# Kernel tuning notes

Hardware: AMD Instinct MI355X
Metric: run time of the kernel (lower is better)

Reference implementation:

```python
import jax, jax.numpy as jnp
import numpy as np

NH = 4  # num_heads
P = 8   # EDFFN patch size


def conv1x1(x, w):
    # x: (B,C,H,W), w: (O,C)
    return jnp.einsum('bchw,oc->bohw', x, w)


def dwconv3x3(x, w):
    # depthwise 3x3, SAME padding. x: (B,C,H,W), w: (C,1,3,3)
    return jax.lax.conv_general_dilated(
        x, w, window_strides=(1, 1), padding='SAME',
        dimension_numbers=('NCHW', 'OIHW', 'NCHW'),
        feature_group_count=x.shape[1])


def affine(x, s, b):
    # folded BatchNorm (eval mode): per-channel scale + bias
    return x * s[None, :, None, None] + b[None, :, None, None]


def setup_inputs() -> dict:
    key = jax.random.key(0)
    ks = jax.random.split(key, 10)
    B, C, H, W = 16, 256, 32, 32
    hd = C // NH              # 64
    kd = hd // 2              # 32 (attn_ratio=0.5)
    h_qkv = C + 2 * kd * NH   # 512
    hid = 2 * C               # EDFFN hidden_features = 512
    x = jax.random.normal(ks[0], (B, C, H, W), dtype=jnp.float32)
    d = {
        'x': x,
        # Attention (ultralytics Conv = conv(no bias) + BN folded to scale/bias)
        'qkv_w': jax.random.normal(ks[1], (h_qkv, C), jnp.float32) * 0.05,
        'qkv_s': jnp.ones((h_qkv,), jnp.float32),
        'qkv_b': jnp.zeros((h_qkv,), jnp.float32),
        'pe_w': jax.random.normal(ks[2], (C, 1, 3, 3), jnp.float32) * 0.1,
        'pe_s': jnp.ones((C,), jnp.float32),
        'pe_b': jnp.zeros((C,), jnp.float32),
        'proj_w': jax.random.normal(ks[3], (C, C), jnp.float32) * 0.05,
        'proj_s': jnp.ones((C,), jnp.float32),
        'proj_b': jnp.zeros((C,), jnp.float32),
        # EDFFN (plain Conv2d, bias=False)
        'pin_w': jax.random.normal(ks[4], (2 * hid, C), jnp.float32) * 0.05,
        'dw_w': jax.random.normal(ks[5], (2 * hid, 1, 3, 3), jnp.float32) * 0.1,
        'fft_filt': jnp.ones((C, 1, 1, P, P // 2 + 1), jnp.float32),
        'pout_w': jax.random.normal(ks[6], (C, hid), jnp.float32) * 0.05,
    }
    return d


def reference(x, qkv_w, qkv_s, qkv_b, pe_w, pe_s, pe_b, proj_w, proj_s, proj_b,
              pin_w, dw_w, fft_filt, pout_w):
    B, C, H, W = x.shape
    hd = C // NH
    kd = hd // 2
    scale = kd ** -0.5
    N = H * W

    # ---- Attention ----
    qkv = affine(conv1x1(x, qkv_w), qkv_s, qkv_b)          # (B, C+2*NH*kd, H, W)
    qkv = qkv.reshape(B, NH, 2 * kd + hd, N)
    q = qkv[:, :, :kd]              # (B, NH, kd, N)
    k = qkv[:, :, kd:2 * kd]        # (B, NH, kd, N)
    v = qkv[:, :, 2 * kd:]          # (B, NH, hd, N)
    attn = jnp.einsum('bhcn,bhcm->bhnm', q, k) * scale     # q^T @ k
    attn = jax.nn.softmax(attn, axis=-1)
    out = jnp.einsum('bhdm,bhnm->bhdn', v, attn)           # v @ attn^T
    out = out.reshape(B, C, H, W)
    v_img = v.reshape(B, C, H, W)
    pe = affine(dwconv3x3(v_img, pe_w), pe_s, pe_b)
    a = affine(conv1x1(out + pe, proj_w), proj_s, proj_b)
    x = x + a                                               # shortcut

    # ---- EDFFN ----
    y = conv1x1(x, pin_w)                                   # (B, 4C, H, W)
    y = dwconv3x3(y, dw_w)
    y1, y2 = jnp.split(y, 2, axis=1)
    y = jax.nn.gelu(y1, approximate=False) * y2             # (B, 2C, H, W)
    y = conv1x1(y, pout_w)                                  # (B, C, H, W)
    h_n = (-H) % P
    w_n = (-W) % P
    if h_n or w_n:
        y = jnp.pad(y, ((0, 0), (0, 0), (0, h_n), (0, w_n)), mode='reflect')
    Hp, Wp = y.shape[2], y.shape[3]
    # (B,C,Hp/P,P,Wp/P,P) -> (B,C,Hp/P,Wp/P,P,P)
    yp = y.reshape(B, C, Hp // P, P, Wp // P, P).transpose(0, 1, 2, 4, 3, 5)
    yf = jnp.fft.rfft2(yp.astype(jnp.float32)) * fft_filt   # filter broadcast (C,1,1,P,P//2+1)
    yp = jnp.fft.irfft2(yf, s=(P, P))
    y = yp.transpose(0, 1, 2, 4, 3, 5).reshape(B, C, Hp, Wp)[:, :, :H, :W]
    return x + y                                            # shortcut
```

## Files before the change

### kernel.cpp

```cpp
#include <hip/hip_runtime.h>
#include <math.h>

#define NPIX 1024

typedef __bf16 bf16x8 __attribute__((ext_vector_type(8)));
typedef float  f32x4  __attribute__((ext_vector_type(4)));

__global__ __launch_bounds__(256) void conv1x1_mfma_kernel(
    const float* __restrict__ in, const float* __restrict__ W,
    const float* __restrict__ sc, const float* __restrict__ bi,
    const float* __restrict__ res, float* __restrict__ out,
    int O, int C) {
  const int b  = blockIdx.z;
  const int o0 = blockIdx.y << 7;
  const int n0 = blockIdx.x << 7;
  const float* inb  = in  + (size_t)b * C * NPIX;
  float*       outb = out + (size_t)b * O * NPIX;
  const float* resb = res ? res + (size_t)b * O * NPIX : nullptr;

  __shared__ __align__(16) __bf16 a_s[128][40];
  __shared__ __align__(16) __bf16 b_s[128][40];

  const int t    = threadIdx.x;
  const int lane = t & 63;
  const int wv   = t >> 6;
  const int wo   = (wv >> 1) << 6;
  const int wn   = (wv & 1) << 6;
  const int lr   = lane & 15;
  const int g    = lane >> 4;

  const int ao = t >> 1, ak = (t & 1) << 4;
  const int bn = t & 127, bk = (t >> 7) << 4;
  const float* wrow = &W[(size_t)(o0 + ao) * C];

  f32x4 acc[4][4];
#pragma unroll
  for (int m = 0; m < 4; ++m)
#pragma unroll
    for (int n = 0; n < 4; ++n) acc[m][n] = (f32x4){0.f, 0.f, 0.f, 0.f};

  for (int k0 = 0; k0 < C; k0 += 32) {
    __syncthreads();
    {
      const float* wp = wrow + k0 + ak;
#pragma unroll
      for (int half = 0; half < 2; ++half) {
        float4 lo = *(const float4*)&wp[half * 8];
        float4 hi = *(const float4*)&wp[half * 8 + 4];
        union { __bf16 h[8]; uint4 u; } pk;
        pk.h[0] = (__bf16)lo.x; pk.h[1] = (__bf16)lo.y;
        pk.h[2] = (__bf16)lo.z; pk.h[3] = (__bf16)lo.w;
        pk.h[4] = (__bf16)hi.x; pk.h[5] = (__bf16)hi.y;
        pk.h[6] = (__bf16)hi.z; pk.h[7] = (__bf16)hi.w;
        *(uint4*)((char*)&a_s[ao][ak] + half * 16) = pk.u;
      }
    }
    {
#pragma unroll
      for (int p = 0; p < 4; ++p) {
        const int kk = k0 + bk + (p << 2);
        union { __bf16 h[4]; uint2 u; } pk;
        pk.h[0] = (__bf16)inb[(size_t)(kk + 0) * NPIX + n0 + bn];
        pk.h[1] = (__bf16)inb[(size_t)(kk + 1) * NPIX + n0 + bn];
        pk.h[2] = (__bf16)inb[(size_t)(kk + 2) * NPIX + n0 + bn];
        pk.h[3] = (__bf16)inb[(size_t)(kk + 3) * NPIX + n0 + bn];
        *(uint2*)((char*)&b_s[bn][bk] + (p << 3)) = pk.u;
      }
    }
    __syncthreads();
    bf16x8 af[4], bfr[4];
#pragma unroll
    for (int m = 0; m < 4; ++m)
      af[m] = *(const bf16x8*)((const char*)&a_s[wo + (m << 4) + lr][0] + (g << 4));
#pragma unroll
    for (int n = 0; n < 4; ++n)
      bfr[n] = *(const bf16x8*)((const char*)&b_s[wn + (n << 4) + lr][0] + (g << 4));
#pragma unroll
    for (int m = 0; m < 4; ++m)
#pragma unroll
      for (int n = 0; n < 4; ++n)
        acc[m][n] = __builtin_amdgcn_mfma_f32_16x16x32_bf16(
            af[m], bfr[n], acc[m][n], 0, 0, 0);
  }

#pragma unroll
  for (int m = 0; m < 4; ++m) {
#pragma unroll
    for (int r = 0; r < 4; ++r) {
      const int o = o0 + wo + (m << 4) + (g << 2) + r;
      const float s  = sc ? sc[o] : 1.f;
      const float bb = bi ? bi[o] : 0.f;
      float* orow = &outb[(size_t)o * NPIX];
      const float* rrow = resb ? &resb[(size_t)o * NPIX] : nullptr;
#pragma unroll
      for (int n = 0; n < 4; ++n) {
        const int nn = n0 + wn + (n << 4) + lr;
        float v = fmaf(acc[m][n][r], s, bb);
        if (rrow) v += rrow[nn];
        orow[nn] = v;
      }
    }
  }
}

__global__ __launch_bounds__(256) void attn_mfma_kernel(
    const float* __restrict__ qkv, float* __restrict__ outbuf) {
  const int L    = blockIdx.x;
  const int xcd  = L & 7;
  const int rrr  = L >> 3;
  const int tile = rrr & 15;
  const int bh   = xcd + ((rrr >> 4) << 3);
  const int h    = bh & 3;
  const int b    = bh >> 2;
  const int n0   = tile << 6;
  const float scale = 0.1767766952966369f;
  const float* base = qkv + ((size_t)b * 512 + h * 128) * NPIX;

  __shared__ __align__(16) char kt_b[64 * 128];
  __shared__ __align__(16) char v_b[64 * 128];
  __shared__ __align__(16) char p_b[4 * 16 * 128];

  const int t    = threadIdx.x;
  const int w    = t >> 6;
  const int lane = t & 63;
  const int lq   = lane & 15;
  const int g    = lane >> 4;

  bf16x8 qf;
  {
    const float* qp = base + (size_t)(g << 3) * NPIX + n0 + (w << 4) + lq;
#pragma unroll
    for (int j = 0; j < 8; ++j)
      qf[j] = (__bf16)(qp[(size_t)j * NPIX] * scale);
  }

  const int cp = t >> 4;
  const int rq = t & 15;
  const float* kr0 = base + (size_t)(32 + (cp << 1)) * NPIX;
  const float* kr1 = kr0 + NPIX;
  const int koff = (cp << 2) ^ ((rq & 7) << 4);
  const int vn = t & 15;
  const int vr = t >> 4;
  const float* vrp = base + (size_t)(64 + vr) * NPIX;

  char* pw = p_b + (w << 11);
  const int pswz = (lq & 7) << 4;

  float m_run = -3.0e38f, l_run = 0.f;
  f32x4 acc0 = {0.f, 0.f, 0.f, 0.f}, acc1 = acc0, acc2 = acc0, acc3 = acc0;

  for (int mt = 0; mt < 16; ++mt) {
    const int m0 = mt << 6;
    __syncthreads();
#pragma unroll
    for (int i = 0; i < 4; ++i) {
      const int m = rq + (i << 4);
      union { __bf16 h2[2]; unsigned u; } pk;
      pk.h2[0] = (__bf16)kr0[m0 + m];
      pk.h2[1] = (__bf16)kr1[m0 + m];
      *(unsigned*)(kt_b + (m << 7) + koff) = pk.u;
    }
#pragma unroll
    for (int i = 0; i < 4; ++i) {
      const int vd = vr + (i << 4);
      float4 v4 = *(const float4*)&vrp[(size_t)(i << 4) * NPIX + m0 + (vn << 2)];
      union { __bf16 h[4]; uint2 u; } pk;
      pk.h[0] = (__bf16)v4.x; pk.h[1] = (__bf16)v4.y;
      pk.h[2] = (__bf16)v4.z; pk.h[3] = (__bf16)v4.w;
      *(uint2*)(v_b + (vd << 7) + ((vn << 3) ^ ((vd & 7) << 4))) = pk.u;
    }
    __syncthreads();

    f32x4 st[4];
#pragma unroll
    for (int tt = 0; tt < 4; ++tt) {
      const int m = (tt << 4) + lq;
      const bf16x8 kfrag = *(const bf16x8*)(
          kt_b + (m << 7) + ((g ^ (lq & 7)) << 4));
      st[tt] = __builtin_amdgcn_mfma_f32_16x16x32_bf16(
          kfrag, qf, (f32x4){0.f, 0.f, 0.f, 0.f}, 0, 0, 0);
    }

    float tmax = -3.0e38f;
#pragma unroll
    for (int tt = 0; tt < 4; ++tt)
#pragma unroll
      for (int r = 0; r < 4; ++r) tmax = fmaxf(tmax, st[tt][r]);
    tmax = fmaxf(tmax, __shfl_xor(tmax, 16));
    tmax = fmaxf(tmax, __shfl_xor(tmax, 32));
    const float mnew  = fmaxf(m_run, tmax);
    const float alpha = __expf(m_run - mnew);
    float ssum = 0.f;
#pragma unroll
    for (int tt = 0; tt < 4; ++tt)
#pragma unroll
      for (int r = 0; r < 4; ++r) {
        st[tt][r] = __expf(st[tt][r] - mnew);
        ssum += st[tt][r];
      }
    ssum += __shfl_xor(ssum, 16);
    ssum += __shfl_xor(ssum, 32);
    l_run = l_run * alpha + ssum;
    m_run = mnew;
    acc0 *= alpha; acc1 *= alpha; acc2 *= alpha; acc3 *= alpha;

#pragma unroll
    for (int tt = 0; tt < 4; ++tt) {
      union { __bf16 h[4]; uint2 u; } pk;
      pk.h[0] = (__bf16)st[tt][0]; pk.h[1] = (__bf16)st[tt][1];
      pk.h[2] = (__bf16)st[tt][2]; pk.h[3] = (__bf16)st[tt][3];
      *(uint2*)(pw + (lq << 7) + (((tt << 5) + (g << 3)) ^ pswz)) = pk.u;
    }

#pragma unroll
    for (int s = 0; s < 2; ++s) {
      const bf16x8 pf = *(const bf16x8*)(
          pw + (lq << 7) + (((s << 6) + (g << 4)) ^ pswz));
      const int cb = ((g << 4) + (s << 6));
#pragma unroll
      for (int dt = 0; dt < 4; ++dt) {
        const int row = (dt << 4) + lq;
        const bf16x8 vfrag = *(const bf16x8*)(
            v_b + (row << 7) + (cb ^ ((lq & 7) << 4)));
        f32x4& a = (dt == 0) ? acc0 : (dt == 1) ? acc1 : (dt == 2) ? acc2 : acc3;
        a = __builtin_amdgcn_mfma_f32_16x16x32_bf16(vfrag, pf, a, 0, 0, 0);
      }
    }
  }

  const float inv = 1.f / l_run;
  float* op = outbuf + ((size_t)b * 256 + h * 64) * NPIX + n0 + (w << 4) + lq;
#pragma unroll
  for (int r = 0; r < 4; ++r) {
    op[(size_t)((0 << 4) + (g << 2) + r) * NPIX] = acc0[r] * inv;
    op[(size_t)((1 << 4) + (g << 2) + r) * NPIX] = acc1[r] * inv;
    op[(size_t)((2 << 4) + (g << 2) + r) * NPIX] = acc2[r] * inv;
    op[(size_t)((3 << 4) + (g << 2) + r) * NPIX] = acc3[r] * inv;
  }
}

__global__ __launch_bounds__(256) void pe_kernel(
    const float* __restrict__ qkv, const float* __restrict__ w,
    const float* __restrict__ s, const float* __restrict__ bi,
    float* __restrict__ att) {
  const int idx = blockIdx.x * 256 + threadIdx.x;
  const int pix = idx & 1023;
  const int ch  = (idx >> 10) & 255;
  const int b   = idx >> 18;
  const int hh = pix >> 5, ww = pix & 31;
  const int row = ((ch >> 6) * 128) + 64 + (ch & 63);
  const float* vimg = qkv + ((size_t)b * 512 + row) * NPIX;
  float acc = 0.f;
#pragma unroll
  for (int dy = -1; dy <= 1; ++dy)
#pragma unroll
    for (int dx = -1; dx <= 1; ++dx) {
      int y = hh + dy, x = ww + dx;
      if (y >= 0 && y < 32 && x >= 0 && x < 32)
        acc = fmaf(w[ch * 9 + (dy + 1) * 3 + (dx + 1)], vimg[(y << 5) + x], acc);
    }
  att[idx] += fmaf(acc, s[ch], bi[ch]);
}

__global__ __launch_bounds__(256) void dwglu_kernel(
    const float* __restrict__ y, const float* __restrict__ w,
    float* __restrict__ g) {
  const int bid = blockIdx.x;
  const int c   = bid & 511;
  const int b   = bid >> 9;

  __shared__ float t1[34 * 34];
  __shared__ float t2[34 * 34];
  const int t = threadIdx.x;

  for (int i = t; i < 34 * 34; i += 256) { t1[i] = 0.f; t2[i] = 0.f; }
  __syncthreads();

  const float* y1 = y + ((size_t)b * 1024 + c) * NPIX;
  const float* y2 = y1 + (size_t)512 * NPIX;
  const int r  = t >> 3;
  const int cq = (t & 7) << 2;
  {
    float4 a1 = *(const float4*)&y1[(r << 5) + cq];
    float4 a2 = *(const float4*)&y2[(r << 5) + cq];
    const int base = (r + 1) * 34 + cq + 1;
    t1[base + 0] = a1.x; t1[base + 1] = a1.y;
    t1[base + 2] = a1.z; t1[base + 3] = a1.w;
    t2[base + 0] = a2.x; t2[base + 1] = a2.y;
    t2[base + 2] = a2.z; t2[base + 3] = a2.w;
  }
  __syncthreads();

  const float* w1 = w + c * 9;
  const float* w2 = w + (512 + c) * 9;
  float W1[9], W2[9];
#pragma unroll
  for (int k = 0; k < 9; ++k) { W1[k] = w1[k]; W2[k] = w2[k]; }

  float4 res;
#pragma unroll
  for (int j = 0; j < 4; ++j) {
    const int x = cq + j;
    float s1 = 0.f, s2 = 0.f;
#pragma unroll
    for (int dy = 0; dy < 3; ++dy)
#pragma unroll
      for (int dx = 0; dx < 3; ++dx) {
        const int idx = (r + dy) * 34 + x + dx;
        const int k   = dy * 3 + dx;
        s1 = fmaf(W1[k], t1[idx], s1);
        s2 = fmaf(W2[k], t2[idx], s2);
      }
    const float ge = 0.5f * s1 * (1.f + erff(s1 * 0.70710678118654752f));
    ((float*)&res)[j] = ge * s2;
  }
  *(float4*)&g[((size_t)b * 512 + c) * NPIX + (r << 5) + cq] = res;
}

__global__ __launch_bounds__(256) void kc_build(
    const float* __restrict__ filt, float* __restrict__ kc) {
  const int gid = blockIdx.x * 256 + threadIdx.x;
  const int c  = gid >> 6;
  const int da = (gid >> 3) & 7;
  const int db = gid & 7;
  const float* F = filt + c * 40;
  float acc = 0.f;
  for (int u = 0; u < 8; ++u)
    for (int v = 0; v <= 4; ++v) {
      const float wv = (v == 0 || v == 4) ? 1.f : 2.f;
      const int ph = (u * da + v * db) & 7;
      acc += wv * F[u * 5 + v] * cosf(0.78539816339744831f * (float)ph);
    }
  kc[gid] = acc * (1.f / 64.f);
}

__global__ __launch_bounds__(256) void fft_final_kernel(
    const float* __restrict__ yin, const float* __restrict__ x2,
    const float* __restrict__ kc, float* __restrict__ out) {
  const int bid = blockIdx.x;
  const int gq = bid & 3;
  const int c  = (bid >> 2) & 255;
  const int b  = bid >> 10;
  __shared__ float kc_s[64];
  __shared__ float tile_s[4][64];
  const int t = threadIdx.x;
  if (t < 64) kc_s[t] = kc[(c << 6) + t];
  const int tl   = t >> 6;
  const int tile = (gq << 2) + tl;
  const int hb = tile >> 2, wb = tile & 3;
  const int a = (t >> 3) & 7, bb2 = t & 7;
  const size_t pbase = ((size_t)b * 256 + c) * NPIX;
  const size_t off = pbase + (size_t)((hb << 3) + a) * 32 + (wb << 3) + bb2;
  tile_s[tl][(a << 3) + bb2] = yin[off];
  __syncthreads();
  float acc = 0.f;
#pragma unroll
  for (int ap = 0; ap < 8; ++ap)
#pragma unroll
    for (int bp = 0; bp < 8; ++bp)
      acc = fmaf(kc_s[(((a - ap) & 7) << 3) + ((bb2 - bp) & 7)],
                 tile_s[tl][(ap << 3) + bp], acc);
  out[off] = x2[off] + acc;
}

extern "C" void kernel_launch(void* const* d_in, const int* in_sizes, int n_in,
                              void* d_out, int out_size, void* d_ws, size_t ws_size,
                              hipStream_t stream) {
  const float* x      = (const float*)d_in[0];
  const float* qkv_w  = (const float*)d_in[1];
  const float* qkv_s  = (const float*)d_in[2];
  const float* qkv_b  = (const float*)d_in[3];
  const float* pe_w   = (const float*)d_in[4];
  const float* pe_s   = (const float*)d_in[5];
  const float* pe_b   = (const float*)d_in[6];
  const float* proj_w = (const float*)d_in[7];
  const float* proj_s = (const float*)d_in[8];
  const float* proj_b = (const float*)d_in[9];
  const float* pin_w  = (const float*)d_in[10];
  const float* dw_w   = (const float*)d_in[11];
  const float* filt   = (const float*)d_in[12];
  const float* pout_w = (const float*)d_in[13];
  float* out = (float*)d_out;
  float* ws  = (float*)d_ws;

  float* qkv_buf = ws;
  float* att_buf = ws + 8388608;
  float* x2      = ws + 12582912;
  float* y_pin   = ws + 16777216;
  float* g_buf   = ws;
  float* y_out   = ws + 8388608;
  float* kc      = ws + 33554432;

  dim3 blk(256);
  kc_build<<<dim3(64), blk, 0, stream>>>(filt, kc);
  conv1x1_mfma_kernel<<<dim3(8, 4, 16), blk, 0, stream>>>(
      x, qkv_w, qkv_s, qkv_b, nullptr, qkv_buf, 512, 256);
  attn_mfma_kernel<<<dim3(1024), blk, 0, stream>>>(qkv_buf, att_buf);
  pe_kernel<<<dim3(16384), blk, 0, stream>>>(qkv_buf, pe_w, pe_s, pe_b, att_buf);
  conv1x1_mfma_kernel<<<dim3(8, 2, 16), blk, 0, stream>>>(
      att_buf, proj_w, proj_s, proj_b, x, x2, 256, 256);
  conv1x1_mfma_kernel<<<dim3(8, 8, 16), blk, 0, stream>>>(
      x2, pin_w, nullptr, nullptr, nullptr, y_pin, 1024, 256);
  dwglu_kernel<<<dim3(8192), blk, 0, stream>>>(y_pin, dw_w, g_buf);
  conv1x1_mfma_kernel<<<dim3(8, 2, 16), blk, 0, stream>>>(
      g_buf, pout_w, nullptr, nullptr, nullptr, y_out, 256, 512);
  fft_final_kernel<<<dim3(16384), blk, 0, stream>>>(y_out, x2, kc, out);
}
```

Before: 306.8 us.

## Process two query tiles per warp in attention to reuse K/V loads

Each attention block now covers 128 query positions instead of 64: every warp holds two query fragments and runs two independent online-softmax streams. Each K/V tile staged in shared memory is therefore used by twice as many queries, which halves the global K/V traffic and conversions and halves the grid. The softmax scale now folds in log2(e) so that exp2f can stand in for __expf. The cost is higher register pressure and a larger P buffer in shared memory, and with only 512 blocks on the GPU occupancy may fall.

```diff
diff --git a/kernel.cpp b/kernel.cpp
--- a/kernel.cpp
+++ b/kernel.cpp
@@ -107,18 +107,18 @@
     const float* __restrict__ qkv, float* __restrict__ outbuf) {
   const int L    = blockIdx.x;
   const int xcd  = L & 7;
-  const int rrr  = L >> 3;
-  const int tile = rrr & 15;
-  const int bh   = xcd + ((rrr >> 4) << 3);
+  const int rr   = L >> 3;
+  const int tile = rr & 7;
+  const int bh   = xcd + ((rr >> 3) << 3);
   const int h    = bh & 3;
   const int b    = bh >> 2;
-  const int n0   = tile << 6;
-  const float scale = 0.1767766952966369f;
+  const int n0   = tile << 7;
+  const float scale2 = 0.25506002427548707f;
   const float* base = qkv + ((size_t)b * 512 + h * 128) * NPIX;
 
   __shared__ __align__(16) char kt_b[64 * 128];
   __shared__ __align__(16) char v_b[64 * 128];
-  __shared__ __align__(16) char p_b[4 * 16 * 128];
+  __shared__ __align__(16) char p_b[4 * 32 * 128];
 
   const int t    = threadIdx.x;
   const int w    = t >> 6;
@@ -126,12 +126,14 @@
   const int lq   = lane & 15;
   const int g    = lane >> 4;
 
-  bf16x8 qf;
+  bf16x8 qfA, qfB;
   {
-    const float* qp = base + (size_t)(g << 3) * NPIX + n0 + (w << 4) + lq;
-#pragma unroll
-    for (int j = 0; j < 8; ++j)
-      qf[j] = (__bf16)(qp[(size_t)j * NPIX] * scale);
+    const float* qp = base + (size_t)(g << 3) * NPIX + n0 + (w << 5) + lq;
+#pragma unroll
+    for (int j = 0; j < 8; ++j) {
+      qfA[j] = (__bf16)(qp[(size_t)j * NPIX] * scale2);
+      qfB[j] = (__bf16)(qp[(size_t)j * NPIX + 16] * scale2);
+    }
   }
 
   const int cp = t >> 4;
@@ -143,11 +145,12 @@
   const int vr = t >> 4;
   const float* vrp = base + (size_t)(64 + vr) * NPIX;
 
-  char* pw = p_b + (w << 11);
+  char* pw = p_b + (w << 12);
   const int pswz = (lq & 7) << 4;
 
-  float m_run = -3.0e38f, l_run = 0.f;
-  f32x4 acc0 = {0.f, 0.f, 0.f, 0.f}, acc1 = acc0, acc2 = acc0, acc3 = acc0;
+  float mA = -3.0e38f, lA = 0.f, mB = -3.0e38f, lB = 0.f;
+  f32x4 accA0 = {0.f, 0.f, 0.f, 0.f}, accA1 = accA0, accA2 = accA0, accA3 = accA0;
+  f32x4 accB0 = accA0, accB1 = accA0, accB2 = accA0, accB3 = accA0;
 
   for (int mt = 0; mt < 16; ++mt) {
     const int m0 = mt << 6;
@@ -171,71 +174,111 @@
     }
     __syncthreads();
 
-    f32x4 st[4];
+    f32x4 stA[4], stB[4];
 #pragma unroll
     for (int tt = 0; tt < 4; ++tt) {
       const int m = (tt << 4) + lq;
       const bf16x8 kfrag = *(const bf16x8*)(
           kt_b + (m << 7) + ((g ^ (lq & 7)) << 4));
-      st[tt] = __builtin_amdgcn_mfma_f32_16x16x32_bf16(
-          kfrag, qf, (f32x4){0.f, 0.f, 0.f, 0.f}, 0, 0, 0);
-    }
-
-    float tmax = -3.0e38f;
-#pragma unroll
-    for (int tt = 0; tt < 4; ++tt)
-#pragma unroll
-      for (int r = 0; r < 4; ++r) tmax = fmaxf(tmax, st[tt][r]);
-    tmax = fmaxf(tmax, __shfl_xor(tmax, 16));
-    tmax = fmaxf(tmax, __shfl_xor(tmax, 32));
-    const float mnew  = fmaxf(m_run, tmax);
-    const float alpha = __expf(m_run - mnew);
-    float ssum = 0.f;
-#pragma unroll
-    for (int tt = 0; tt < 4; ++tt)
-#pragma unroll
-      for (int r = 0; r < 4; ++r) {
-        st[tt][r] = __expf(st[tt][r] - mnew);
-        ssum += st[tt][r];
-      }
-    ssum += __shfl_xor(ssum, 16);
-    ssum += __shfl_xor(ssum, 32);
-    l_run = l_run * alpha + ssum;
-    m_run = mnew;
-    acc0 *= alpha; acc1 *= alpha; acc2 *= alpha; acc3 *= alpha;
+      stA[tt] = __builtin_amdgcn_mfma_f32_16x16x32_bf16(
+          kfrag, qfA, (f32x4){0.f, 0.f, 0.f, 0.f}, 0, 0, 0);
+      stB[tt] = __builtin_amdgcn_mfma_f32_16x16x32_bf16(
+          kfrag, qfB, (f32x4){0.f, 0.f, 0.f, 0.f}, 0, 0, 0);
+    }
+
+    {
+      float tmax = -3.0e38f;
+#pragma unroll
+      for (int tt = 0; tt < 4; ++tt)
+#pragma unroll
+        for (int r = 0; r < 4; ++r) tmax = fmaxf(tmax, stA[tt][r]);
+      tmax = fmaxf(tmax, __shfl_xor(tmax, 16));
+      tmax = fmaxf(tmax, __shfl_xor(tmax, 32));
+      const float mnew  = fmaxf(mA, tmax);
+      const float alpha = exp2f(mA - mnew);
+      float ssum = 0.f;
+#pragma unroll
+      for (int tt = 0; tt < 4; ++tt)
+#pragma unroll
+        for (int r = 0; r < 4; ++r) {
+          stA[tt][r] = exp2f(stA[tt][r] - mnew);
+          ssum += stA[tt][r];
+        }
+      ssum += __shfl_xor(ssum, 16);
+      ssum += __shfl_xor(ssum, 32);
+      lA = lA * alpha + ssum;
+      mA = mnew;
+      accA0 *= alpha; accA1 *= alpha; accA2 *= alpha; accA3 *= alpha;
+    }
+    {
+      float tmax = -3.0e38f;
+#pragma unroll
+      for (int tt = 0; tt < 4; ++tt)
+#pragma unroll
+        for (int r = 0; r < 4; ++r) tmax = fmaxf(tmax, stB[tt][r]);
+      tmax = fmaxf(tmax, __shfl_xor(tmax, 16));
+      tmax = fmaxf(tmax, __shfl_xor(tmax, 32));
+      const float mnew  = fmaxf(mB, tmax);
+      const float alpha = exp2f(mB - mnew);
+      float ssum = 0.f;
+#pragma unroll
+      for (int tt = 0; tt < 4; ++tt)
+#pragma unroll
+        for (int r = 0; r < 4; ++r) {
+          stB[tt][r] = exp2f(stB[tt][r] - mnew);
+          ssum += stB[tt][r];
+        }
+      ssum += __shfl_xor(ssum, 16);
+      ssum += __shfl_xor(ssum, 32);
+      lB = lB * alpha + ssum;
+      mB = mnew;
+      accB0 *= alpha; accB1 *= alpha; accB2 *= alpha; accB3 *= alpha;
+    }
 
 #pragma unroll
     for (int tt = 0; tt < 4; ++tt) {
-      union { __bf16 h[4]; uint2 u; } pk;
-      pk.h[0] = (__bf16)st[tt][0]; pk.h[1] = (__bf16)st[tt][1];
-      pk.h[2] = (__bf16)st[tt][2]; pk.h[3] = (__bf16)st[tt][3];
-      *(uint2*)(pw + (lq << 7) + (((tt << 5) + (g << 3)) ^ pswz)) = pk.u;
+      union { __bf16 h[4]; uint2 u; } pkA, pkB;
+      pkA.h[0] = (__bf16)stA[tt][0]; pkA.h[1] = (__bf16)stA[tt][1];
+      pkA.h[2] = (__bf16)stA[tt][2]; pkA.h[3] = (__bf16)stA[tt][3];
+      pkB.h[0] = (__bf16)stB[tt][0]; pkB.h[1] = (__bf16)stB[tt][1];
+      pkB.h[2] = (__bf16)stB[tt][2]; pkB.h[3] = (__bf16)stB[tt][3];
+      const int cbyte = ((tt << 5) + (g << 3)) ^ pswz;
+      *(uint2*)(pw + (lq << 7) + cbyte) = pkA.u;
+      *(uint2*)(pw + ((lq + 16) << 7) + cbyte) = pkB.u;
     }
 
 #pragma unroll
     for (int s = 0; s < 2; ++s) {
-      const bf16x8 pf = *(const bf16x8*)(
-          pw + (lq << 7) + (((s << 6) + (g << 4)) ^ pswz));
+      const int cbyte = ((s << 6) + (g << 4)) ^ pswz;
+      const bf16x8 pfA = *(const bf16x8*)(pw + (lq << 7) + cbyte);
+      const bf16x8 pfB = *(const bf16x8*)(pw + ((lq + 16) << 7) + cbyte);
       const int cb = ((g << 4) + (s << 6));
 #pragma unroll
       for (int dt = 0; dt < 4; ++dt) {
         const int row = (dt << 4) + lq;
         const bf16x8 vfrag = *(const bf16x8*)(
             v_b + (row << 7) + (cb ^ ((lq & 7) << 4)));
-        f32x4& a = (dt == 0) ? acc0 : (dt == 1) ? acc1 : (dt == 2) ? acc2 : acc3;
-        a = __builtin_amdgcn_mfma_f32_16x16x32_bf16(vfrag, pf, a, 0, 0, 0);
+        f32x4& aA = (dt == 0) ? accA0 : (dt == 1) ? accA1 : (dt == 2) ? accA2 : accA3;
+        f32x4& aB = (dt == 0) ? accB0 : (dt == 1) ? accB1 : (dt == 2) ? accB2 : accB3;
+        aA = __builtin_amdgcn_mfma_f32_16x16x32_bf16(vfrag, pfA, aA, 0, 0, 0);
+        aB = __builtin_amdgcn_mfma_f32_16x16x32_bf16(vfrag, pfB, aB, 0, 0, 0);
       }
     }
   }
 
-  const float inv = 1.f / l_run;
-  float* op = outbuf + ((size_t)b * 256 + h * 64) * NPIX + n0 + (w << 4) + lq;
+  const float invA = 1.f / lA, invB = 1.f / lB;
+  float* opA = outbuf + ((size_t)b * 256 + h * 64) * NPIX + n0 + (w << 5) + lq;
+  float* opB = opA + 16;
 #pragma unroll
   for (int r = 0; r < 4; ++r) {
-    op[(size_t)((0 << 4) + (g << 2) + r) * NPIX] = acc0[r] * inv;
-    op[(size_t)((1 << 4) + (g << 2) + r) * NPIX] = acc1[r] * inv;
-    op[(size_t)((2 << 4) + (g << 2) + r) * NPIX] = acc2[r] * inv;
-    op[(size_t)((3 << 4) + (g << 2) + r) * NPIX] = acc3[r] * inv;
+    opA[(size_t)(( 0) + (g << 2) + r) * NPIX] = accA0[r] * invA;
+    opA[(size_t)((16) + (g << 2) + r) * NPIX] = accA1[r] * invA;
+    opA[(size_t)((32) + (g << 2) + r) * NPIX] = accA2[r] * invA;
+    opA[(size_t)((48) + (g << 2) + r) * NPIX] = accA3[r] * invA;
+    opB[(size_t)(( 0) + (g << 2) + r) * NPIX] = accB0[r] * invB;
+    opB[(size_t)((16) + (g << 2) + r) * NPIX] = accB1[r] * invB;
+    opB[(size_t)((32) + (g << 2) + r) * NPIX] = accB2[r] * invB;
+    opB[(size_t)((48) + (g << 2) + r) * NPIX] = accB3[r] * invB;
   }
 }
 
@@ -395,7 +438,7 @@
   kc_build<<<dim3(64), blk, 0, stream>>>(filt, kc);
   conv1x1_mfma_kernel<<<dim3(8, 4, 16), blk, 0, stream>>>(
       x, qkv_w, qkv_s, qkv_b, nullptr, qkv_buf, 512, 256);
-  attn_mfma_kernel<<<dim3(1024), blk, 0, stream>>>(qkv_buf, att_buf);
+  attn_mfma_kernel<<<dim3(512), blk, 0, stream>>>(qkv_buf, att_buf);
   pe_kernel<<<dim3(16384), blk, 0, stream>>>(qkv_buf, pe_w, pe_s, pe_b, att_buf);
   conv1x1_mfma_kernel<<<dim3(8, 2, 16), blk, 0, stream>>>(
       att_buf, proj_w, proj_s, proj_b, x, x2, 256, 256);
```

Result: slower. 314.2 us (+2.4%).
